# Optimization experiments

Hardware: AMD Instinct MI355X
Metric: run time of the kernel (lower is better)

The kernel has to match this reference:

```python
import jax, jax.numpy as jnp
import numpy as np

VMF_KAPPA = 30.0      # vMF concentration
THRESHOLD = 0.0       # vc_thresholds
OCC_LIKELY = 0.6      # occ_likely[0]
NUM_MIXTURES = 4
EPS_L1 = 1e-12        # torch F.normalize eps


def _l1_normalize(x, axis):
    n = jnp.sum(jnp.abs(x), axis=axis, keepdims=True)
    return x / jnp.maximum(n, EPS_L1)


def _crop_or_pad(mm, H, W):
    # center crop or zero-pad mix model spatial dims to (H, W); shapes are static
    _, _, hm, wm = mm.shape
    if hm < H:
        d1 = (H - hm) // 2
        mm = jnp.pad(mm, ((0, 0), (0, 0), (d1, H - hm - d1), (0, 0)))
    elif hm > H:
        d1 = (hm - H) // 2
        mm = mm[:, :, d1:d1 + H, :]
    if wm < W:
        d1 = (W - wm) // 2
        mm = jnp.pad(mm, ((0, 0), (0, 0), (0, 0), (d1, W - wm - d1)))
    elif wm > W:
        d1 = (wm - W) // 2
        mm = mm[:, :, :, d1:d1 + W]
    return mm


def setup_inputs() -> dict:
    key = jax.random.key(0)
    k1, k2, k3, k4 = jax.random.split(key, 4)
    B, C, H, W = 32, 512, 56, 56
    VC = 512              # number of vMF codebook vectors
    KM = 48               # num_classes(12) * num_mixtures(4)
    NCLUT = 5             # clutter models
    return {
        "vgg_feat": jax.random.normal(k1, (B, C, H, W), dtype=jnp.float32),
        "conv_weight": jax.random.normal(k2, (VC, C, 1, 1), dtype=jnp.float32),
        "mix_model": jax.random.uniform(k3, (KM, VC, H, W), dtype=jnp.float32),
        "clutter_model": jax.random.uniform(k4, (NCLUT, VC), dtype=jnp.float32),
    }


def reference(vgg_feat, conv_weight, mix_model, clutter_model):
    B, C, H, W = vgg_feat.shape
    # --- Conv1o1: cosine similarity between L2-normalized features and codebook ---
    xnorm = jnp.linalg.norm(vgg_feat, axis=1, keepdims=True)
    xnorm = xnorm + (xnorm == 0).astype(vgg_feat.dtype)  # avoid div-by-zero
    xn = vgg_feat / xnorm
    w = conv_weight[:, :, 0, 0]                           # (vc, C) 1x1 kernel
    wn = w / jnp.linalg.norm(w, axis=1, keepdims=True)
    cos = jnp.einsum('bchw,kc->bkhw', xn, wn)             # (B, vc, H, W)
    # --- vMF activation ---
    act = jnp.exp(VMF_KAPPA * cos) * (cos > THRESHOLD).astype(cos.dtype)
    # --- PointwiseInferenceLayer (vmf, use_mixture_bg=True) ---
    ck = _l1_normalize(jnp.clip(clutter_model, 0.0, 1.0), axis=1)  # (N, vc)
    bg = jnp.einsum('bkhw,nk->bnhw', act, ck)                      # (B, N, H, W)
    background = jnp.log(bg * OCC_LIKELY + 1e-10)
    background = jnp.max(background, axis=1, keepdims=True)        # (B, 1, H, W)
    background = background[:, None, None]                         # (B,1,1,1,H,W)

    mm = _l1_normalize(jnp.clip(mix_model, 0.0, 1.0), axis=1)      # (KM, vc, Hm, Wm)
    mm = _crop_or_pad(mm, H, W)
    fg = jnp.einsum('bkhw,mkhw->bmhw', act, mm)                    # (B, KM, H, W)
    foreground = jnp.log(fg * (1.0 - OCC_LIKELY) + 1e-10)
    num_classes = mm.shape[0] // NUM_MIXTURES
    foreground = foreground.reshape(B, num_classes, NUM_MIXTURES, 1, H, W)
    per_model = jnp.maximum(foreground, background).sum(axis=(-1, -2))  # (B,K,M,1)
    scores = per_model.max(axis=-1).max(axis=-1)                        # (B, K)
    mix_likeli = scores / (H * W)
    # SoftMaxTemp(2.0)
    z = jnp.exp(jnp.clip(mix_likeli * 2.0, -88.7, 88.7))
    soft = z / jnp.sum(z, axis=1, keepdims=True)
    return soft, vgg_feat, mix_likeli
```

## Files before the change

kernel.cpp:

```cpp
#include <hip/hip_runtime.h>

#define B_ 32
#define C_ 512
#define HW_ 3136
#define KF_ 512
#define KM_ 48
#define NCL_ 5

typedef __attribute__((ext_vector_type(8))) short short8;
typedef __attribute__((ext_vector_type(4))) short short4v;
typedef __attribute__((ext_vector_type(4))) float floatx4;
typedef unsigned int u32;
typedef u32 __attribute__((address_space(1))) gu32;
typedef u32 __attribute__((address_space(3))) lu32;

__device__ __forceinline__ unsigned short f2bf(float f) {
    union { float f; unsigned u; } v; v.f = f;
    unsigned r = v.u + 0x7FFFu + ((v.u >> 16) & 1u);
    return (unsigned short)(r >> 16);
}
__device__ __forceinline__ void gl2lds16(const void* g, void* l) {
    __builtin_amdgcn_global_load_lds((const gu32*)g, (lu32*)l, 16, 0, 0);
}

__global__ __launch_bounds__(64) void prep_kernel(const float* __restrict__ w,
                                                  const float* __restrict__ cl,
                                                  unsigned short* __restrict__ wn,
                                                  float* __restrict__ ck) {
    int bid = blockIdx.x, t = threadIdx.x;
    if (bid < KF_) {
        const float* row = w + (size_t)bid * C_;
        float ss = 0.f;
        float x[8];
#pragma unroll
        for (int j = 0; j < 8; ++j) { x[j] = row[t * 8 + j]; ss += x[j] * x[j]; }
        for (int m = 32; m >= 1; m >>= 1) ss += __shfl_xor(ss, m);
        float inv = 1.f / sqrtf(ss);
#pragma unroll
        for (int j = 0; j < 8; ++j) wn[(size_t)bid * C_ + t * 8 + j] = f2bf(x[j] * inv);
    } else {
        int n = bid - KF_;
        if (n >= NCL_) return;
        const float* row = cl + (size_t)n * KF_;
        float s = 0.f;
        float v[8];
#pragma unroll
        for (int j = 0; j < 8; ++j) {
            float x = row[t * 8 + j];
            x = fminf(fmaxf(x, 0.f), 1.f);
            v[j] = x; s += x;
        }
        for (int m = 32; m >= 1; m >>= 1) s += __shfl_xor(s, m);
        float inv = 1.f / fmaxf(s, 1e-12f);
#pragma unroll
        for (int j = 0; j < 8; ++j) ck[(size_t)n * KF_ + t * 8 + j] = v[j] * inv;
    }
}

__global__ __launch_bounds__(512) void xprep_kernel(const float* __restrict__ vgg,
                                                    unsigned short* __restrict__ xnt,
                                                    float* __restrict__ invn,
                                                    float* __restrict__ out_vgg,
                                                    int write_vgg) {
    int pt = blockIdx.x, b = blockIdx.y;
    int tid = threadIdx.x;
    int px = tid & 63, cq = tid >> 6;
    __shared__ __align__(16) unsigned short tile[64][512];
    __shared__ float ssp[8][64];
    const float* vcol = vgg + (size_t)b * C_ * HW_ + pt * 64 + px;
    float* ovcol = out_vgg + (size_t)b * C_ * HW_ + pt * 64 + px;

    float ss = 0.f;
#pragma unroll
    for (int j = 0; j < 16; ++j) {
        int c0 = cq * 64 + j * 4;
        float x0 = vcol[(size_t)(c0 + 0) * HW_];
        float x1 = vcol[(size_t)(c0 + 1) * HW_];
        float x2 = vcol[(size_t)(c0 + 2) * HW_];
        float x3 = vcol[(size_t)(c0 + 3) * HW_];
        ss += x0 * x0 + x1 * x1 + x2 * x2 + x3 * x3;
        short4v pk;
        pk[0] = (short)f2bf(x0); pk[1] = (short)f2bf(x1);
        pk[2] = (short)f2bf(x2); pk[3] = (short)f2bf(x3);
        *(short4v*)&tile[px][c0] = pk;
        if (write_vgg) {
            ovcol[(size_t)(c0 + 0) * HW_] = x0;
            ovcol[(size_t)(c0 + 1) * HW_] = x1;
            ovcol[(size_t)(c0 + 2) * HW_] = x2;
            ovcol[(size_t)(c0 + 3) * HW_] = x3;
        }
    }
    ssp[cq][px] = ss;
    __syncthreads();
    if (tid < 64) {
        float s = 0.f;
#pragma unroll
        for (int q = 0; q < 8; ++q) s += ssp[q][tid];
        float n = sqrtf(s);
        invn[(size_t)b * HW_ + pt * 64 + tid] = (n == 0.f) ? 1.f : 1.f / n;
    }
    __syncthreads();
    int row = tid >> 3, ch = tid & 7;
    unsigned short* orow = xnt + ((size_t)b * HW_ + pt * 64 + row) * 512;
#pragma unroll
    for (int j = 0; j < 8; ++j) {
        int c8 = (ch + 8 * j) * 8;
        *(short8*)(orow + c8) = *(const short8*)&tile[row][c8];
    }
}

__global__ __launch_bounds__(512) void gemm_act_kernel(const unsigned short* __restrict__ xnt,
                                                       const unsigned short* __restrict__ wn,
                                                       const float* __restrict__ invn,
                                                       const float* __restrict__ ck,
                                                       unsigned short* __restrict__ act,
                                                       float* __restrict__ bgacc) {
    int wg = blockIdx.x;
    int swz = (wg & 7) * 392 + (wg >> 3);
    int pt = swz >> 2, ft = swz & 3;
    int tid = threadIdx.x, lane = tid & 63;
    int wid = tid >> 6;
    int li = lane & 15, q = lane >> 4;
    int wm = wid & 1, wq = wid >> 1;

    __shared__ __align__(16) unsigned short a_lds[2][128 * 64];
    __shared__ __align__(16) unsigned short b_lds[2][128 * 64];
    __shared__ float inv_l[128];
    __shared__ float ck_l[NCL_ * KF_];
    __shared__ float bga_l[128 * NCL_];
    if (tid < 128) inv_l[tid] = invn[(size_t)pt * 128 + tid];
    for (int i = tid; i < NCL_ * KF_; i += 512) ck_l[i] = ck[i];
    for (int i = tid; i < 128 * NCL_; i += 512) bga_l[i] = 0.f;

    const unsigned short* ga = wn + ((size_t)ft * 128 + (tid >> 3)) * 512 + (tid & 7) * 8;
    const unsigned short* gb = xnt + ((size_t)pt * 128 + (tid >> 3)) * 512 + (tid & 7) * 8;
    int ldst = tid * 8;

    floatx4 acc[4][2] = {};

#pragma unroll
    for (int i = 0; i < 2; ++i) {
        gl2lds16(ga + (size_t)i * 64 * 512, &a_lds[0][ldst + i * 4096]);
        gl2lds16(gb + (size_t)i * 64 * 512, &b_lds[0][ldst + i * 4096]);
    }

#pragma unroll 1
    for (int s = 0; s < 8; ++s) {
        __builtin_amdgcn_s_barrier();
        if (s < 7) {
            int nb = (s + 1) & 1;
#pragma unroll
            for (int i = 0; i < 2; ++i) {
                gl2lds16(ga + (size_t)i * 64 * 512 + (s + 1) * 64, &a_lds[nb][ldst + i * 4096]);
                gl2lds16(gb + (size_t)i * 64 * 512 + (s + 1) * 64, &b_lds[nb][ldst + i * 4096]);
            }
            asm volatile("s_waitcnt vmcnt(4)" ::: "memory");
        } else {
            asm volatile("s_waitcnt vmcnt(0)" ::: "memory");
        }
        __builtin_amdgcn_sched_barrier(0);
        __builtin_amdgcn_s_barrier();
        int buf = s & 1;
#pragma unroll
        for (int k2 = 0; k2 < 2; ++k2) {
            short8 af[4], bfr[2];
#pragma unroll
            for (int i = 0; i < 4; ++i)
                af[i] = *(const short8*)&a_lds[buf][(wm * 64 + i * 16 + li) * 64 + k2 * 32 + q * 8];
#pragma unroll
            for (int j = 0; j < 2; ++j)
                bfr[j] = *(const short8*)&b_lds[buf][(wq * 32 + j * 16 + li) * 64 + k2 * 32 + q * 8];
#pragma unroll
            for (int i = 0; i < 4; ++i)
#pragma unroll
                for (int j = 0; j < 2; ++j)
                    acc[i][j] = __builtin_amdgcn_mfma_f32_16x16x32_bf16(af[i], bfr[j], acc[i][j], 0, 0, 0);
        }
    }

#pragma unroll
    for (int j = 0; j < 2; ++j) {
        int px = wq * 32 + j * 16 + li;
        float inv = inv_l[px];
        size_t row_g = (size_t)pt * 128 + px;
        float bp[NCL_] = {0.f, 0.f, 0.f, 0.f, 0.f};
#pragma unroll
        for (int i = 0; i < 4; ++i) {
            int chn = ft * 8 + wm * 4 + i;
            int f_g = ft * 128 + wm * 64 + i * 16 + q * 4;
            short4v pk;
            float av[4];
#pragma unroll
            for (int r = 0; r < 4; ++r) {
                float cv = acc[i][j][r] * inv;
                float a = cv > 0.f ? __expf(30.f * cv) : 0.f;
                av[r] = a;
                pk[r] = (short)f2bf(a);
            }
            *(short4v*)(act + ((size_t)chn * 100352 + row_g) * 16 + q * 4) = pk;
#pragma unroll
            for (int n = 0; n < NCL_; ++n)
                bp[n] += av[0] * ck_l[n * KF_ + f_g] + av[1] * ck_l[n * KF_ + f_g + 1] +
                         av[2] * ck_l[n * KF_ + f_g + 2] + av[3] * ck_l[n * KF_ + f_g + 3];
        }
#pragma unroll
        for (int n = 0; n < NCL_; ++n) {
            float v = bp[n];
            v += __shfl_xor(v, 16);
            v += __shfl_xor(v, 32);
            if (q == 0) atomicAdd(&bga_l[px * NCL_ + n], v);
        }
    }
    __syncthreads();
    if (tid < 128) {
        size_t row_g = (size_t)pt * 128 + tid;
#pragma unroll
        for (int n = 0; n < NCL_; ++n)
            atomicAdd(&bgacc[row_g * 8 + n], bga_l[tid * NCL_ + n]);
    }
}

__global__ __launch_bounds__(512) void fg3_kernel(const unsigned short* __restrict__ act,
                                                  const float* __restrict__ mm,
                                                  const float* __restrict__ bgacc,
                                                  float* __restrict__ pm) {
    __shared__ __align__(16) unsigned char L[145408];
    float* bgs    = (float*)(L + 131072);
    float* csum_s = (float*)(L + 139264);
    float* pms    = (float*)(L + 143360);

    int bid = blockIdx.x;
    int xcd = bid & 7, rest = bid >> 3;
    int mg = rest % 3, ptq = rest / 3;
    int pt = xcd + 8 * ptq;
    if (pt >= 49) return;
    int px0 = pt * 64;
    int m0 = mg * 16;

    int tid = threadIdx.x;
    int lane = tid & 63, w = tid >> 6;
    int li = lane & 15, q = lane >> 4;
    int w8 = w * 8;

    pms[tid & 511] = 0.f;
    for (int i = tid; i < 2048; i += 512) {
        int b = i >> 6, p = i & 63;
        const float* bgp = bgacc + ((size_t)b * HW_ + px0 + p) * 8;
        float mx = -1e30f;
#pragma unroll
        for (int n = 0; n < NCL_; ++n) mx = fmaxf(mx, logf(bgp[n] * 0.6f + 1e-10f));
        bgs[i] = mx;
    }

    const unsigned short* srcA[4];
    int dA[4];
#pragma unroll
    for (int t = 0; t < 4; ++t) {
        int b = w * 4 + t;
        srcA[t] = act + ((size_t)b * HW_ + px0 + (lane ^ (b & 7))) * 16;
        dA[t] = b * 1024 + lane * 16;
    }
    const float* srcM[2][2];
    int dM[2][2];
#pragma unroll
    for (int u = 0; u < 2; ++u)
#pragma unroll
        for (int kq = 0; kq < 2; ++kq) {
            int m = w * 2 + u;
            int k = kq * 4 + (lane >> 4);
            int g = (lane & 15) ^ m;
            srcM[u][kq] = mm + ((size_t)(m0 + m) * KF_ + k) * HW_ + px0 + g * 4;
            dM[u][kq] = m * 2048 + kq * 1024 + lane * 16;
        }

    auto stage = [&](int s) {
        unsigned char* base = L + (size_t)(s & 1) * 65536;
#pragma unroll
        for (int t = 0; t < 4; ++t)
            gl2lds16(srcA[t] + (size_t)(s >> 1) * 1605632 + (s & 1) * 8, base + dA[t]);
#pragma unroll
        for (int u = 0; u < 2; ++u)
#pragma unroll
            for (int kq = 0; kq < 2; ++kq)
                gl2lds16(srcM[u][kq] + (size_t)s * 8 * HW_, base + 32768 + dM[u][kq]);
    };

    short8 fA[8], fb0[8], fb1[8];
    floatx4 acc0[8] = {}, acc1[8] = {};
    float csp[8] = {0.f, 0.f, 0.f, 0.f, 0.f, 0.f, 0.f, 0.f};

    stage(0);

#pragma unroll 4
    for (int s = 0; s < 64; ++s) {
        __builtin_amdgcn_s_barrier();
        if (s < 63) {
            stage(s + 1);
            asm volatile("s_waitcnt vmcnt(8)" ::: "memory");
        } else {
            asm volatile("s_waitcnt vmcnt(0)" ::: "memory");
        }
        __builtin_amdgcn_sched_barrier(0);
        __builtin_amdgcn_s_barrier();
        const unsigned char* ab = L + (size_t)(s & 1) * 65536;
        const unsigned char* mb = ab + 32768;
        int rq = s & 3;
        if (q == rq) {
#pragma unroll
            for (int e = 0; e < 8; ++e) {
                int p = w8 + e;
                int slotA = (p ^ (li & 7)) * 16;
                fb0[e] = *(const short8*)(ab + li * 1024 + slotA);
                fb1[e] = *(const short8*)(ab + (16 + li) * 1024 + slotA);
                const unsigned char* mrow = mb + li * 2048 +
                                            ((((p >> 2) ^ li) & 15) * 16) + (p & 3) * 4;
                short8 pk;
                float cs = 0.f;
#pragma unroll
                for (int k = 0; k < 8; ++k) {
                    float x = *(const float*)(mrow + k * 256);
                    x = fminf(fmaxf(x, 0.f), 1.f);
                    cs += x;
                    pk[k] = (short)f2bf(x);
                }
                csp[e] += cs;
                fA[e] = pk;
            }
        }
        if (rq == 3) {
#pragma unroll
            for (int e = 0; e < 8; ++e) {
                acc0[e] = __builtin_amdgcn_mfma_f32_16x16x32_bf16(fA[e], fb0[e], acc0[e], 0, 0, 0);
                acc1[e] = __builtin_amdgcn_mfma_f32_16x16x32_bf16(fA[e], fb1[e], acc1[e], 0, 0, 0);
            }
        }
    }

#pragma unroll
    for (int e = 0; e < 8; ++e) {
        float v = csp[e];
        v += __shfl_xor(v, 16);
        v += __shfl_xor(v, 32);
        if (q == 0) csum_s[li * 64 + w8 + e] = v;
    }
    __syncthreads();

#pragma unroll
    for (int bf = 0; bf < 2; ++bf) {
        int b = bf * 16 + li;
#pragma unroll
        for (int r = 0; r < 4; ++r) {
            int ml = q * 4 + r;
            float sacc = 0.f;
#pragma unroll
            for (int e = 0; e < 8; ++e) {
                int p = w8 + e;
                float inv = 1.f / fmaxf(csum_s[ml * 64 + p], 1e-12f);
                float a = (bf == 0) ? acc0[e][r] : acc1[e][r];
                sacc += fmaxf(logf(a * inv * 0.4f + 1e-10f), bgs[b * 64 + p]);
            }
            atomicAdd(&pms[ml * 32 + b], sacc);
        }
    }
    __syncthreads();
    {
        int ml = tid >> 5, b = tid & 31;
        atomicAdd(&pm[(size_t)b * KM_ + m0 + ml], pms[tid]);
    }
}

__global__ __launch_bounds__(64) void final_kernel(const float* __restrict__ pm,
                                                   float* __restrict__ out_soft,
                                                   float* __restrict__ out_ml) {
    int b = threadIdx.x;
    if (b >= B_) return;
    float ml[12];
#pragma unroll
    for (int c = 0; c < 12; ++c) {
        float s = -1e30f;
#pragma unroll
        for (int j = 0; j < 4; ++j) s = fmaxf(s, pm[(size_t)b * KM_ + c * 4 + j]);
        ml[c] = s / (float)HW_;
    }
    float z[12], zs = 0.f;
#pragma unroll
    for (int c = 0; c < 12; ++c) {
        float e = fminf(fmaxf(ml[c] * 2.f, -88.7f), 88.7f);
        z[c] = expf(e); zs += z[c];
    }
#pragma unroll
    for (int c = 0; c < 12; ++c) {
        out_soft[(size_t)b * 12 + c] = z[c] / zs;
        out_ml[(size_t)b * 12 + c] = ml[c];
    }
}

extern "C" void kernel_launch(void* const* d_in, const int* in_sizes, int n_in,
                              void* d_out, int out_size, void* d_ws, size_t ws_size,
                              hipStream_t stream) {
    const float* vgg = (const float*)d_in[0];
    const float* cw  = (const float*)d_in[1];
    const float* mmp = (const float*)d_in[2];
    const float* cl  = (const float*)d_in[3];
    float* out = (float*)d_out;
    char* ws = (char*)d_ws;

    unsigned short* wn   = (unsigned short*)(ws);
    float* ck            = (float*)(ws + 524288);
    float* invn          = (float*)(ws + 534528);
    float* pm            = (float*)(ws + 935936);
    float* bgacc         = (float*)(ws + 942080);
    unsigned short* xnt  = (unsigned short*)(ws + 4153344);
    const size_t ACT_OFF = 4153344 + 102760448;
    const size_t ACT_BYTES = (size_t)B_ * HW_ * KF_ * 2;

    int act_in_ws = (ws_size >= ACT_OFF + ACT_BYTES) ? 1 : 0;
    unsigned short* act = act_in_ws ? (unsigned short*)(ws + ACT_OFF)
                                    : (unsigned short*)(out + 384);

    hipMemsetAsync(pm, 0, (size_t)B_ * KM_ * sizeof(float), stream);
    hipMemsetAsync(bgacc, 0, (size_t)B_ * HW_ * 8 * sizeof(float), stream);
    prep_kernel<<<dim3(KF_ + NCL_), dim3(64), 0, stream>>>(cw, cl, wn, ck);
    xprep_kernel<<<dim3(49, 32), dim3(512), 0, stream>>>(vgg, xnt, invn, out + 384, act_in_ws);
    gemm_act_kernel<<<dim3(3136), dim3(512), 0, stream>>>(xnt, wn, invn, ck, act, bgacc);
    fg3_kernel<<<dim3(168), dim3(512), 0, stream>>>(act, mmp, bgacc, pm);
    final_kernel<<<1, 64, 0, stream>>>(pm, out, out + 384 + (size_t)B_ * C_ * HW_);
    if (!act_in_ws)
        hipMemcpyAsync(out + 384, vgg, (size_t)B_ * C_ * HW_ * sizeof(float),
                       hipMemcpyDeviceToDevice, stream);
}
```

Measured before the change: 451.9 us.

## Rewrite foreground kernel with smaller tiles, register-staged loads and higher occupancy

Replaces fg3 with fg4. Tiles shrink to 32 pixels x 16 mixtures x 16 batches, giving 588 blocks with an XCD-aware index mapping instead of 168. Direct global-to-LDS loads are replaced by register prefetch, and the mix-model clamp and bf16 conversion now happen once at LDS write time rather than per reader. LDS per block drops to about 70KB and launch bounds request more resident blocks, aiming to raise occupancy and latency hiding. The cost is that each mix-model tile is re-read by both batch halves and the atomic reduction traffic grows.

```diff
diff --git a/kernel.cpp b/kernel.cpp
--- a/kernel.cpp
+++ b/kernel.cpp
@@ -220,152 +220,133 @@
     }
 }
 
-__global__ __launch_bounds__(512) void fg3_kernel(const unsigned short* __restrict__ act,
-                                                  const float* __restrict__ mm,
-                                                  const float* __restrict__ bgacc,
-                                                  float* __restrict__ pm) {
-    __shared__ __align__(16) unsigned char L[145408];
-    float* bgs    = (float*)(L + 131072);
-    float* csum_s = (float*)(L + 139264);
-    float* pms    = (float*)(L + 143360);
+#define FG4_MML 0
+#define FG4_ACTL 32768
+#define FG4_BGS 65536
+#define FG4_CSUM 67584
+#define FG4_PMS 69632
+__global__ __launch_bounds__(512, 4) void fg4_kernel(const unsigned short* __restrict__ act,
+                                                     const float* __restrict__ mm,
+                                                     const float* __restrict__ bgacc,
+                                                     float* __restrict__ pm) {
+    __shared__ __align__(16) unsigned char L[70656];
+    float* bgs    = (float*)(L + FG4_BGS);
+    float* csum_s = (float*)(L + FG4_CSUM);
+    float* pms    = (float*)(L + FG4_PMS);
 
     int bid = blockIdx.x;
-    int xcd = bid & 7, rest = bid >> 3;
-    int mg = rest % 3, ptq = rest / 3;
-    int pt = xcd + 8 * ptq;
-    if (pt >= 49) return;
-    int px0 = pt * 64;
-    int m0 = mg * 16;
+    int xcd = bid & 7, pos = bid >> 3;
+    int linear = (xcd < 4 ? xcd * 74 : 296 + (xcd - 4) * 73) + pos;
+    int pt = linear / 6, sub = linear - pt * 6;
+    int mg = sub >> 1, bh = sub & 1;
+    int p0 = pt * 32, m0 = mg * 16, b0 = bh * 16;
 
     int tid = threadIdx.x;
     int lane = tid & 63, w = tid >> 6;
     int li = lane & 15, q = lane >> 4;
-    int w8 = w * 8;
-
-    pms[tid & 511] = 0.f;
-    for (int i = tid; i < 2048; i += 512) {
-        int b = i >> 6, p = i & 63;
-        const float* bgp = bgacc + ((size_t)b * HW_ + px0 + p) * 8;
+
+    if (tid < 256) pms[tid] = 0.f;
+    csum_s[tid] = 0.f;
+    {
+        int b = tid >> 5, px = tid & 31;
+        const float* bgp = bgacc + ((size_t)(b0 + b) * HW_ + p0 + px) * 8;
         float mx = -1e30f;
 #pragma unroll
         for (int n = 0; n < NCL_; ++n) mx = fmaxf(mx, logf(bgp[n] * 0.6f + 1e-10f));
-        bgs[i] = mx;
-    }
-
-    const unsigned short* srcA[4];
-    int dA[4];
-#pragma unroll
-    for (int t = 0; t < 4; ++t) {
-        int b = w * 4 + t;
-        srcA[t] = act + ((size_t)b * HW_ + px0 + (lane ^ (b & 7))) * 16;
-        dA[t] = b * 1024 + lane * 16;
-    }
-    const float* srcM[2][2];
-    int dM[2][2];
-#pragma unroll
-    for (int u = 0; u < 2; ++u)
-#pragma unroll
-        for (int kq = 0; kq < 2; ++kq) {
-            int m = w * 2 + u;
-            int k = kq * 4 + (lane >> 4);
-            int g = (lane & 15) ^ m;
-            srcM[u][kq] = mm + ((size_t)(m0 + m) * KF_ + k) * HW_ + px0 + g * 4;
-            dM[u][kq] = m * 2048 + kq * 1024 + lane * 16;
-        }
-
-    auto stage = [&](int s) {
-        unsigned char* base = L + (size_t)(s & 1) * 65536;
-#pragma unroll
-        for (int t = 0; t < 4; ++t)
-            gl2lds16(srcA[t] + (size_t)(s >> 1) * 1605632 + (s & 1) * 8, base + dA[t]);
-#pragma unroll
-        for (int u = 0; u < 2; ++u)
-#pragma unroll
-            for (int kq = 0; kq < 2; ++kq)
-                gl2lds16(srcM[u][kq] + (size_t)s * 8 * HW_, base + 32768 + dM[u][kq]);
+        bgs[b * 32 + px] = mx;
+    }
+
+    int ab = tid >> 5, apx = tid & 31;
+    int mmM = tid >> 5, mkq = (tid >> 3) & 3, mpxg = tid & 7;
+    const unsigned short* aSrc = act + ((size_t)(b0 + ab) * HW_ + p0 + apx) * 16;
+    const float* mSrc = mm + ((size_t)(m0 + mmM) * KF_ + mkq * 4) * HW_ + p0 + mpxg * 4;
+    unsigned char* aW = L + FG4_ACTL + ab * 1024 + ((apx ^ (ab & 3)) * 32);
+
+    floatx4 mr[4];
+    short8 ar[2];
+    float cs[4] = {0.f, 0.f, 0.f, 0.f};
+    floatx4 acc[4] = {};
+    short8 fa[4], fb[4];
+
+    auto loadRegs = [&](int s) {
+#pragma unroll
+        for (int j = 0; j < 4; ++j)
+            mr[j] = *(const floatx4*)(mSrc + ((size_t)s * 16 + j) * HW_);
+        const unsigned short* as = aSrc + (size_t)s * 1605632;
+        ar[0] = *(const short8*)(as);
+        ar[1] = *(const short8*)(as + 8);
     };
-
-    short8 fA[8], fb0[8], fb1[8];
-    floatx4 acc0[8] = {}, acc1[8] = {};
-    float csp[8] = {0.f, 0.f, 0.f, 0.f, 0.f, 0.f, 0.f, 0.f};
-
-    stage(0);
-
-#pragma unroll 4
-    for (int s = 0; s < 64; ++s) {
-        __builtin_amdgcn_s_barrier();
-        if (s < 63) {
-            stage(s + 1);
-            asm volatile("s_waitcnt vmcnt(8)" ::: "memory");
-        } else {
-            asm volatile("s_waitcnt vmcnt(0)" ::: "memory");
-        }
-        __builtin_amdgcn_sched_barrier(0);
-        __builtin_amdgcn_s_barrier();
-        const unsigned char* ab = L + (size_t)(s & 1) * 65536;
-        const unsigned char* mb = ab + 32768;
-        int rq = s & 3;
-        if (q == rq) {
-#pragma unroll
-            for (int e = 0; e < 8; ++e) {
-                int p = w8 + e;
-                int slotA = (p ^ (li & 7)) * 16;
-                fb0[e] = *(const short8*)(ab + li * 1024 + slotA);
-                fb1[e] = *(const short8*)(ab + (16 + li) * 1024 + slotA);
-                const unsigned char* mrow = mb + li * 2048 +
-                                            ((((p >> 2) ^ li) & 15) * 16) + (p & 3) * 4;
-                short8 pk;
-                float cs = 0.f;
-#pragma unroll
-                for (int k = 0; k < 8; ++k) {
-                    float x = *(const float*)(mrow + k * 256);
-                    x = fminf(fmaxf(x, 0.f), 1.f);
-                    cs += x;
-                    pk[k] = (short)f2bf(x);
-                }
-                csp[e] += cs;
-                fA[e] = pk;
+    auto cvtWrite = [&](int s) {
+        int buf = (s & 1) * 16384;
+#pragma unroll
+        for (int i = 0; i < 4; ++i) {
+            int px = mpxg * 4 + i;
+            float x0 = fminf(fmaxf(mr[0][i], 0.f), 1.f);
+            float x1 = fminf(fmaxf(mr[1][i], 0.f), 1.f);
+            float x2 = fminf(fmaxf(mr[2][i], 0.f), 1.f);
+            float x3 = fminf(fmaxf(mr[3][i], 0.f), 1.f);
+            cs[i] += x0 + x1 + x2 + x3;
+            short4v pk;
+            pk[0] = (short)f2bf(x0); pk[1] = (short)f2bf(x1);
+            pk[2] = (short)f2bf(x2); pk[3] = (short)f2bf(x3);
+            *(short4v*)(L + FG4_MML + buf + mmM * 1024 + ((px ^ (mmM & 3)) * 32) + mkq * 8) = pk;
+        }
+        *(short8*)(aW + buf) = ar[0];
+        *(short8*)(aW + buf + 16) = ar[1];
+    };
+
+    loadRegs(0);
+    cvtWrite(0);
+    loadRegs(1);
+    __syncthreads();
+
+#pragma unroll 2
+    for (int s = 0; s < 32; ++s) {
+        const unsigned char* bufM = L + FG4_MML + (s & 1) * 16384;
+        const unsigned char* bufA = L + FG4_ACTL + (s & 1) * 16384;
+        if ((q >> 1) == (s & 1)) {
+#pragma unroll
+            for (int e = 0; e < 4; ++e) {
+                int px = w * 4 + e;
+                int off = li * 1024 + ((px ^ (li & 3)) * 32) + (q & 1) * 16;
+                fa[e] = *(const short8*)(bufM + off);
+                fb[e] = *(const short8*)(bufA + off);
             }
         }
-        if (rq == 3) {
-#pragma unroll
-            for (int e = 0; e < 8; ++e) {
-                acc0[e] = __builtin_amdgcn_mfma_f32_16x16x32_bf16(fA[e], fb0[e], acc0[e], 0, 0, 0);
-                acc1[e] = __builtin_amdgcn_mfma_f32_16x16x32_bf16(fA[e], fb1[e], acc1[e], 0, 0, 0);
-            }
-        }
-    }
-
-#pragma unroll
-    for (int e = 0; e < 8; ++e) {
-        float v = csp[e];
-        v += __shfl_xor(v, 16);
-        v += __shfl_xor(v, 32);
-        if (q == 0) csum_s[li * 64 + w8 + e] = v;
-    }
-    __syncthreads();
-
-#pragma unroll
-    for (int bf = 0; bf < 2; ++bf) {
-        int b = bf * 16 + li;
-#pragma unroll
-        for (int r = 0; r < 4; ++r) {
-            int ml = q * 4 + r;
-            float sacc = 0.f;
-#pragma unroll
-            for (int e = 0; e < 8; ++e) {
-                int p = w8 + e;
-                float inv = 1.f / fmaxf(csum_s[ml * 64 + p], 1e-12f);
-                float a = (bf == 0) ? acc0[e][r] : acc1[e][r];
-                sacc += fmaxf(logf(a * inv * 0.4f + 1e-10f), bgs[b * 64 + p]);
-            }
-            atomicAdd(&pms[ml * 32 + b], sacc);
-        }
-    }
-    __syncthreads();
-    {
-        int ml = tid >> 5, b = tid & 31;
-        atomicAdd(&pm[(size_t)b * KM_ + m0 + ml], pms[tid]);
+        if (s & 1) {
+#pragma unroll
+            for (int e = 0; e < 4; ++e)
+                acc[e] = __builtin_amdgcn_mfma_f32_16x16x32_bf16(fa[e], fb[e], acc[e], 0, 0, 0);
+        }
+        if (s < 31) {
+            cvtWrite(s + 1);
+            if (s < 30) loadRegs(s + 2);
+        }
+        __syncthreads();
+    }
+
+#pragma unroll
+    for (int i = 0; i < 4; ++i)
+        atomicAdd(&csum_s[mmM * 32 + mpxg * 4 + i], cs[i]);
+    __syncthreads();
+
+#pragma unroll
+    for (int r = 0; r < 4; ++r) {
+        int m = q * 4 + r;
+        float sacc = 0.f;
+#pragma unroll
+        for (int e = 0; e < 4; ++e) {
+            int px = w * 4 + e;
+            float inv = 1.f / fmaxf(csum_s[m * 32 + px], 1e-12f);
+            float v = fmaxf(logf(acc[e][r] * inv * 0.4f + 1e-10f), bgs[li * 32 + px]);
+            sacc += v;
+        }
+        atomicAdd(&pms[m * 16 + li], sacc);
+    }
+    __syncthreads();
+    if (tid < 256) {
+        int m = tid >> 4, b = tid & 15;
+        atomicAdd(&pm[(size_t)(b0 + b) * KM_ + m0 + m], pms[m * 16 + b]);
     }
 }
 
@@ -423,7 +404,7 @@
     prep_kernel<<<dim3(KF_ + NCL_), dim3(64), 0, stream>>>(cw, cl, wn, ck);
     xprep_kernel<<<dim3(49, 32), dim3(512), 0, stream>>>(vgg, xnt, invn, out + 384, act_in_ws);
     gemm_act_kernel<<<dim3(3136), dim3(512), 0, stream>>>(xnt, wn, invn, ck, act, bgacc);
-    fg3_kernel<<<dim3(168), dim3(512), 0, stream>>>(act, mmp, bgacc, pm);
+    fg4_kernel<<<dim3(588), dim3(512), 0, stream>>>(act, mmp, bgacc, pm);
     final_kernel<<<1, 64, 0, stream>>>(pm, out, out + 384 + (size_t)B_ * C_ * HW_);
     if (!act_in_ws)
         hipMemcpyAsync(out + 384, vgg, (size_t)B_ * C_ * HW_ * sizeof(float),
```

Measured after the change: 402.2 us, median of 2. -11.0%, faster.
